# Performance work log

Measured on AMD Instinct MI355X. Metric: run time of the kernel, lower is better.

Reference implementation:

```python
import jax, jax.numpy as jnp
import numpy as np

B, L, C = 16, 2048, 1024
H, G, K = 16, 4, 5
GC = C // G          # group channels = 256
DH = C // H          # head channels = 64
PAD = K // 2         # 2


def conv1d(x, w, b, pad):
    # x: [N, Cin, L], w: [Cout, Cin, K]
    out = jax.lax.conv_general_dilated(x, w, (1,), [(pad, pad)],
                                       dimension_numbers=('NCH', 'OIH', 'NCH'))
    return out + b[None, :, None]


def setup_inputs() -> dict:
    key = jax.random.key(0)
    ks = jax.random.split(key, 16)
    s = 0.02
    inp = {
        'x': jax.random.normal(ks[0], (B, L, C), jnp.float32),
        'Wq': jax.random.normal(ks[1], (C, C), jnp.float32) * s,
        'bq': jnp.zeros((C,), jnp.float32),
        'Wk': jax.random.normal(ks[2], (C, C), jnp.float32) * s,
        'bk': jnp.zeros((C,), jnp.float32),
        'Wv': jax.random.normal(ks[3], (C, C), jnp.float32) * s,
        'bv': jnp.zeros((C,), jnp.float32),
        'Woff1': jax.random.normal(ks[4], (GC, GC, K), jnp.float32) * s,
        'boff1': jnp.zeros((GC,), jnp.float32),
        'Woff2': jax.random.normal(ks[5], (1, GC, 1), jnp.float32) * s,
        'boff2': jnp.zeros((1,), jnp.float32),
        'rpb_table': jax.random.normal(ks[6], (1, C, L), jnp.float32) * 0.02,
        'Wout': jax.random.normal(ks[7], (C, C), jnp.float32) * s,
        'bout': jnp.zeros((C,), jnp.float32),
    }
    return inp


def reference(x, Wq, bq, Wk, bk, Wv, bv, Woff1, boff1, Woff2, boff2,
              rpb_table, Wout, bout):
    xT = jnp.swapaxes(x, 1, 2)                        # [B, C, L]
    # conv1x1 q projection
    q = jnp.einsum('oc,bcl->bol', Wq, xT) + bq[None, :, None]
    gq = q.reshape(B * G, GC, L)                       # grouped queries
    # offset network: conv(k=5, pad=2) -> conv(k=1, pad=2) => length L+4
    h = conv1d(gq, Woff1, boff1, PAD)                  # [BG, GC, L]
    off = conv1d(h, Woff2, boff2, PAD)                 # [BG, 1, L+4]
    off = jnp.tanh(off[:, 0, :]) * K                   # offset_range_factor = kernel
    L4 = L + 2 * PAD
    grid = jnp.arange(L4, dtype=x.dtype)
    vgrid = grid[None, :] + off                        # [BG, L4]
    vs = 2.0 * vgrid / (L4 - 1) - 1.0                  # normalize with n = L+4 (as in source)
    # grid_sample bilinear, align_corners=False, zeros padding, over length L
    pos = ((vs + 1.0) * L - 1.0) / 2.0
    i0 = jnp.floor(pos)
    w1 = pos - i0
    i0 = i0.astype(jnp.int32)
    feats = xT.reshape(B * G, GC, L)

    def gather(idx):
        valid = ((idx >= 0) & (idx < L)).astype(x.dtype)
        idxc = jnp.clip(idx, 0, L - 1)
        g = jnp.take_along_axis(feats, jnp.broadcast_to(idxc[:, None, :], (B * G, GC, L4)), axis=2)
        return g * valid[:, None, :]

    samp = gather(i0) * (1.0 - w1)[:, None, :] + gather(i0 + 1) * w1[:, None, :]
    x_sampled = samp[:, :, :L].reshape(B, C, L)

    k = jnp.einsum('oc,bcl->bol', Wk, x_sampled) + bk[None, :, None]
    v = jnp.einsum('oc,bcl->bol', Wv, x_sampled) + bv[None, :, None] + rpb_table

    qh = q.reshape(B * H, DH, L)
    kh = k.reshape(B * H, DH, L)
    vh = v.reshape(B * H, DH, L)
    # attention over head-channel dims, contracting over sequence (faithful to source)
    scores = jnp.einsum('bil,bjl->bij', qh, kh) * (C ** -0.5)   # [BH, DH, DH]
    attn = jax.nn.softmax(scores, axis=-1)
    out = jnp.einsum('bij,bjl->bil', attn, vh)                  # [BH, DH, L]
    # rearrange '(b g) l c -> b c (g l)' with b=B, g=H, l=DH, c=L
    out = out.reshape(B, H, DH, L).transpose(0, 3, 1, 2).reshape(B, L, C)
    return out @ Wout.T + bout
```

## Files before the change

kernel.cpp:

```cpp
#include <hip/hip_runtime.h>
#include <hip/hip_bf16.h>
#include <stdint.h>

#define BATCH 16
#define SEQ   2048
#define CH    1024
#define NH    16
#define NG    4
#define KW    5
#define GCH   256
#define DHD   64
#define NBG   (BATCH*NG)
#define NBH   (BATCH*NH)
#define MROWS (BATCH*SEQ)

typedef __hip_bfloat16 bf16;
typedef float f32x4 __attribute__((ext_vector_type(4)));
typedef __bf16 bf16x8 __attribute__((ext_vector_type(8)));

__device__ __forceinline__ void unpack8(uint4 r, float* f){
    uint32_t w0=r.x,w1=r.y,w2=r.z,w3=r.w;
    f[0]=__uint_as_float(w0<<16); f[1]=__uint_as_float(w0&0xffff0000u);
    f[2]=__uint_as_float(w1<<16); f[3]=__uint_as_float(w1&0xffff0000u);
    f[4]=__uint_as_float(w2<<16); f[5]=__uint_as_float(w2&0xffff0000u);
    f[6]=__uint_as_float(w3<<16); f[7]=__uint_as_float(w3&0xffff0000u);
}

__global__ __launch_bounds__(256)
void cvt_kernel(const float* __restrict__ in, bf16* __restrict__ out, int n)
{
    int i = (blockIdx.x*256 + threadIdx.x)*8;
    if (i >= n) return;
    float4 f0 = *(const float4*)(in+i);
    float4 f1 = *(const float4*)(in+i+4);
    union { bf16 b[8]; uint4 u; } pk;
    pk.b[0]=__float2bfloat16(f0.x); pk.b[1]=__float2bfloat16(f0.y);
    pk.b[2]=__float2bfloat16(f0.z); pk.b[3]=__float2bfloat16(f0.w);
    pk.b[4]=__float2bfloat16(f1.x); pk.b[5]=__float2bfloat16(f1.y);
    pk.b[6]=__float2bfloat16(f1.z); pk.b[7]=__float2bfloat16(f1.w);
    *(uint4*)(out+i) = pk.u;
}

__global__ void prep_weff_kernel(const float* __restrict__ W1, const float* __restrict__ b1,
                                 const float* __restrict__ w2, const float* __restrict__ b2,
                                 float* __restrict__ weff, float* __restrict__ wcst)
{
    int kk = blockIdx.x;
    int cj = threadIdx.x;
    float s = 0.f;
    for (int co=0; co<GCH; ++co)
        s += w2[co] * W1[((size_t)co*GCH + cj)*KW + kk];
    weff[kk*GCH + cj] = s;
    if (kk==0 && cj==0){
        float sb = 0.f;
        for (int co=0; co<GCH; ++co) sb += w2[co]*b1[co];
        wcst[0] = b2[0];
        wcst[1] = sb;
    }
}

template<int MODE>
__global__ __launch_bounds__(512, 2)
void gemm256_kernel(const bf16* __restrict__ A, const bf16* __restrict__ Wb,
                    const float* __restrict__ bias, const float* __restrict__ rpb,
                    void* __restrict__ outp)
{
    __shared__ __bf16 SM[2*32768];
    const int t = threadIdx.x;
    const int w = t>>6, l = t&63;
    const int wrow = w>>2, wcol = w&3;
    const int lr = l&15, kq = l>>4;

    const int lin = blockIdx.x;
    const int xcd = lin&7, sblk = lin>>3;
    const int m0 = (xcd*16 + (sblk>>2))*256;
    const int n0 = (sblk&3)*256;

    const bf16* Ag = A  + (size_t)m0*CH;
    const bf16* Bg = Wb + (size_t)n0*CH;

    int srow[4], scol[4];
    #pragma unroll
    for (int r=0;r<4;++r){
        int o = (t + 512*r)*16;
        int e = o ^ (((o>>7)&7)<<4);
        srow[r] = e>>7;
        scol[r] = (e&127)>>1;
    }

    auto STAGE = [&](int tile, int buf){
        const int kt = tile*64;
        __bf16* ab = SM + buf*32768;
        __bf16* bb = ab + 16384;
        #pragma unroll
        for (int r=0;r<4;++r){
            __builtin_amdgcn_global_load_lds(
                (const __attribute__((address_space(1))) void*)(Ag + (size_t)srow[r]*CH + kt + scol[r]),
                (__attribute__((address_space(3))) void*)(ab + w*512 + r*4096), 16, 0, 0);
            __builtin_amdgcn_global_load_lds(
                (const __attribute__((address_space(1))) void*)(Bg + (size_t)srow[r]*CH + kt + scol[r]),
                (__attribute__((address_space(3))) void*)(bb + w*512 + r*4096), 16, 0, 0);
        }
    };

    f32x4 acc[8][4];
    #pragma unroll
    for (int i=0;i<8;++i)
        #pragma unroll
        for (int j=0;j<4;++j) acc[i][j] = (f32x4){0.f,0.f,0.f,0.f};

    STAGE(0, 0);
    asm volatile("s_waitcnt vmcnt(0)" ::: "memory");
    __builtin_amdgcn_s_barrier();
    __builtin_amdgcn_sched_barrier(0);

    const int NT = CH/64;
    for (int tt=0; tt<NT; ++tt){
        const int cur = tt&1;
        if (tt+1 < NT) STAGE(tt+1, cur^1);
        __builtin_amdgcn_sched_barrier(0);

        const __bf16* As_ = SM + cur*32768;
        const __bf16* Bs_ = As_ + 16384;
        #pragma unroll
        for (int ks=0; ks<2; ++ks){
            bf16x8 af[8], bfr[4];
            #pragma unroll
            for (int fi=0; fi<8; ++fi){
                int row = wrow*128 + fi*16 + lr;
                int byte = row*128 + ks*64 + kq*16;
                byte ^= (row&7)<<4;
                af[fi] = *(const bf16x8*)(As_ + (byte>>1));
            }
            #pragma unroll
            for (int fj=0; fj<4; ++fj){
                int row = wcol*64 + fj*16 + lr;
                int byte = row*128 + ks*64 + kq*16;
                byte ^= (row&7)<<4;
                bfr[fj] = *(const bf16x8*)(Bs_ + (byte>>1));
            }
            asm volatile("s_waitcnt lgkmcnt(0)" ::: "memory");
            __builtin_amdgcn_sched_barrier(0);
            __builtin_amdgcn_s_setprio(1);
            #pragma unroll
            for (int fi=0; fi<8; ++fi)
                #pragma unroll
                for (int fj=0; fj<4; ++fj)
                    acc[fi][fj] = __builtin_amdgcn_mfma_f32_16x16x32_bf16(af[fi], bfr[fj], acc[fi][fj], 0,0,0);
            __builtin_amdgcn_s_setprio(0);
        }
        asm volatile("s_waitcnt vmcnt(0)" ::: "memory");
        __builtin_amdgcn_s_barrier();
        __builtin_amdgcn_sched_barrier(0);
    }

    float bs[4];
    #pragma unroll
    for (int fj=0;fj<4;++fj) bs[fj] = bias[n0 + wcol*64 + fj*16 + lr];

    if constexpr (MODE == 2){
        const int bb2 = m0 >> 11;
        const int l0g = m0 & (SEQ-1);
        bf16* outT = (bf16*)outp;
        #pragma unroll
        for (int fi=0; fi<8; ++fi){
            int rowl = wrow*128 + fi*16 + kq*4;
            #pragma unroll
            for (int fj=0; fj<4; ++fj){
                int col = n0 + wcol*64 + fj*16 + lr;
                union { bf16 h[4]; uint2 u; } pk;
                #pragma unroll
                for (int r=0;r<4;++r) pk.h[r] = __float2bfloat16(acc[fi][fj][r] + bs[fj]);
                *(uint2*)(outT + ((size_t)(bb2*CH + col))*SEQ + l0g + rowl) = pk.u;
            }
        }
    } else {
        #pragma unroll
        for (int fi=0; fi<8; ++fi){
            #pragma unroll
            for (int r=0;r<4;++r){
                int mg = m0 + wrow*128 + fi*16 + kq*4 + r;
                int lseq = mg & (SEQ-1);
                #pragma unroll
                for (int fj=0; fj<4; ++fj){
                    int ng = n0 + wcol*64 + fj*16 + lr;
                    float v = acc[fi][fj][r] + bs[fj];
                    if constexpr (MODE==1) v += rpb[(size_t)ng*SEQ + lseq];
                    if constexpr (MODE==3)
                        ((float*)outp)[(size_t)mg*CH + ng] = v;
                    else
                        ((bf16*)outp)[(size_t)mg*CH + ng] = __float2bfloat16(v);
                }
            }
        }
    }
}

__global__ __launch_bounds__(256)
void offsets_kernel(const bf16* __restrict__ QT, const float* __restrict__ weff,
                    const float* __restrict__ wcst, float* __restrict__ posb)
{
    __shared__ float P5R[8][272][5];
    __shared__ float weffL[KW][GCH];
    const int t = threadIdx.x;
    const int chunk = blockIdx.x, bg = blockIdx.y;
    const int b = bg>>2, g = bg&3;
    const int l0 = chunk*256;

    for (int i = t; i < KW*GCH; i += 256) weffL[i>>8][i&255] = weff[i];
    __syncthreads();

    const int jg = t & 31, cg = t >> 5;

    auto doblock = [&](int jb, int cgx){
        const int j0 = l0 - 8 + jb*8;
        float acc[8][KW];
        #pragma unroll
        for (int e=0;e<8;++e)
            #pragma unroll
            for (int kk=0;kk<KW;++kk) acc[e][kk] = 0.f;
        const bf16* base = QT + ((size_t)(b*CH + g*GCH + cgx*32))*SEQ;
        const bool safe = (j0 >= 0) && (j0 + 8 <= SEQ);
        if (safe){
            #pragma unroll 4
            for (int i=0;i<32;++i){
                float xv[8];
                { union { bf16x8 v; uint4 u; } cv;
                  cv.v = *(const bf16x8*)(base + (size_t)i*SEQ + j0);
                  unpack8(cv.u, xv); }
                float wk[KW];
                #pragma unroll
                for (int kk=0;kk<KW;++kk) wk[kk] = weffL[kk][cgx*32 + i];
                #pragma unroll
                for (int e=0;e<8;++e)
                    #pragma unroll
                    for (int kk=0;kk<KW;++kk) acc[e][kk] += xv[e]*wk[kk];
            }
        } else {
            for (int i=0;i<32;++i){
                float wk[KW];
                #pragma unroll
                for (int kk=0;kk<KW;++kk) wk[kk] = weffL[kk][cgx*32 + i];
                #pragma unroll
                for (int e=0;e<8;++e){
                    int j = j0 + e;
                    float xv = (j >= 0 && j < SEQ)
                             ? __bfloat162float(base[(size_t)i*SEQ + j]) : 0.f;
                    #pragma unroll
                    for (int kk=0;kk<KW;++kk) acc[e][kk] += xv*wk[kk];
                }
            }
        }
        #pragma unroll
        for (int e=0;e<8;++e)
            #pragma unroll
            for (int kk=0;kk<KW;++kk) P5R[cgx][jb*8+e][kk] = acc[e][kk];
    };

    doblock(jg, cg);
    if (t < 16) doblock(32 + (t&1), t>>1);
    __syncthreads();

    const int lp = l0 + t;
    const float b2 = wcst[0], wb1 = wcst[1];
    float o;
    if (lp < 2){
        o = b2;
    } else {
        float s = b2 + wb1;
        #pragma unroll
        for (int kk=0;kk<KW;++kk){
            int j = lp - 4 + kk;
            if (j >= 0 && j < SEQ){
                int jp = t + 4 + kk;
                float v = 0.f;
                #pragma unroll
                for (int c8=0;c8<8;++c8) v += P5R[c8][jp][kk];
                s += v;
            }
        }
        o = s;
    }
    float off = tanhf(o) * (float)KW;
    posb[bg*SEQ + lp] = ((float)lp + off) * (2048.0f/2051.0f) - 0.5f;
}

__global__ __launch_bounds__(256)
void sample_kernel(const bf16* __restrict__ Xbf, const float* __restrict__ posb,
                   bf16* __restrict__ XS)
{
    const int ci = threadIdx.x, bg = blockIdx.y;
    const int b = bg>>2, g = bg&3;
    const int lp0 = blockIdx.x*8;
    #pragma unroll
    for (int s8=0; s8<8; ++s8){
        int lp = lp0 + s8;
        float p  = posb[bg*SEQ + lp];
        float fl = floorf(p);
        float w1 = p - fl;
        int i0 = (int)fl;
        float v = 0.f;
        if (i0 >= 0 && i0 < SEQ)
            v += __bfloat162float(Xbf[((size_t)(b*SEQ + i0))*CH + g*GCH + ci]) * (1.f - w1);
        if (i0+1 >= 0 && i0+1 < SEQ)
            v += __bfloat162float(Xbf[((size_t)(b*SEQ + i0 + 1))*CH + g*GCH + ci]) * w1;
        XS[((size_t)(b*SEQ + lp))*CH + g*GCH + ci] = __float2bfloat16(v);
    }
}

__global__ __launch_bounds__(256)
void attn_s_kernel(const bf16* __restrict__ QT, const bf16* __restrict__ KT,
                   bf16* __restrict__ Pbuf)
{
    __shared__ float Sc[64][69];
    __shared__ float red[64][4];
    __shared__ float mrow[64];
    __shared__ float sinv[64];
    const int t = threadIdx.x, w = t>>6, l = t&63;
    const int bh = blockIdx.x, b = bh>>4, h = bh&15;
    const bf16* q = QT + ((size_t)(b*CH + h*DHD))*SEQ;
    const bf16* k = KT + ((size_t)(b*CH + h*DHD))*SEQ;
    const int lr = l&15, lk = (l>>4)*8;

    f32x4 acc[4][4];
    #pragma unroll
    for (int i=0;i<4;++i)
        #pragma unroll
        for (int j=0;j<4;++j) acc[i][j] = (f32x4){0.f,0.f,0.f,0.f};

    for (int ks=0; ks<16; ++ks){
        int kp = w*512 + ks*32 + lk;
        bf16x8 af[4], bk8[4];
        #pragma unroll
        for (int i=0;i<4;++i) af[i]  = *(const bf16x8*)(q + (size_t)(i*16+lr)*SEQ + kp);
        #pragma unroll
        for (int j=0;j<4;++j) bk8[j] = *(const bf16x8*)(k + (size_t)(j*16+lr)*SEQ + kp);
        #pragma unroll
        for (int i=0;i<4;++i)
            #pragma unroll
            for (int j=0;j<4;++j)
                acc[i][j] = __builtin_amdgcn_mfma_f32_16x16x32_bf16(af[i], bk8[j], acc[i][j], 0,0,0);
    }
    for (int wv=0; wv<4; ++wv){
        if (w == wv){
            #pragma unroll
            for (int i=0;i<4;++i)
                #pragma unroll
                for (int j=0;j<4;++j)
                    #pragma unroll
                    for (int r=0;r<4;++r){
                        int m = i*16 + (l>>4)*4 + r, n = j*16 + lr;
                        if (wv==0) Sc[m][n]  = acc[i][j][r];
                        else       Sc[m][n] += acc[i][j][r];
                    }
        }
        __syncthreads();
    }
    const int r0 = t & 63, p = t >> 6;
    const float SCALE = 0.03125f;
    float mx = -1e30f;
    #pragma unroll
    for (int c=0;c<16;++c) mx = fmaxf(mx, Sc[r0][p*16+c]*SCALE);
    red[r0][p] = mx;
    __syncthreads();
    if (t < 64) mrow[t] = fmaxf(fmaxf(red[t][0],red[t][1]), fmaxf(red[t][2],red[t][3]));
    __syncthreads();
    float m = mrow[r0], s = 0.f;
    #pragma unroll
    for (int c=0;c<16;++c){
        float e = expf(Sc[r0][p*16+c]*SCALE - m);
        Sc[r0][p*16+c] = e;
        s += e;
    }
    red[r0][p] = s;
    __syncthreads();
    if (t < 64) sinv[t] = 1.f/(red[t][0]+red[t][1]+red[t][2]+red[t][3]);
    __syncthreads();
    float inv = sinv[r0];
    union { bf16 b[8]; uint4 u; } p0, p1;
    #pragma unroll
    for (int e=0;e<8;++e){
        p0.b[e] = __float2bfloat16(Sc[r0][p*16+e]*inv);
        p1.b[e] = __float2bfloat16(Sc[r0][p*16+8+e]*inv);
    }
    bf16* dst = Pbuf + (size_t)bh*4096 + r0*64 + p*16;
    *(uint4*)dst       = p0.u;
    *(uint4*)(dst + 8) = p1.u;
}

__global__ __launch_bounds__(256)
void attn_pv_kernel(const bf16* __restrict__ Pbuf, const bf16* __restrict__ V,
                    bf16* __restrict__ F)
{
    __shared__ __bf16 Pl[64][72];
    const int t = threadIdx.x, w = t>>6, l = t&63;
    const int chunk = blockIdx.x, bh = blockIdx.y;
    const int b = bh>>4, h = bh&15;
    {
        int row = t>>2, coff = (t&3)*16;
        const bf16* src = Pbuf + (size_t)bh*4096 + row*64 + coff;
        *(uint4*)&Pl[row][coff]   = *(const uint4*)src;
        *(uint4*)&Pl[row][coff+8] = *(const uint4*)(src+8);
    }
    __syncthreads();
    const int lr = l&15, lk = (l>>4)*8;
    const int lw = chunk*256 + w*64;

    f32x4 acc[4][4];
    #pragma unroll
    for (int i=0;i<4;++i)
        #pragma unroll
        for (int j=0;j<4;++j) acc[i][j] = (f32x4){0.f,0.f,0.f,0.f};

    #pragma unroll
    for (int ks=0; ks<2; ++ks){
        bf16x8 pf[4], vf[4];
        #pragma unroll
        for (int ni=0;ni<4;++ni) pf[ni] = *(const bf16x8*)&Pl[ni*16+lr][ks*32+lk];
        #pragma unroll
        for (int mi=0;mi<4;++mi)
            vf[mi] = *(const bf16x8*)(V + ((size_t)(b*SEQ + lw + mi*16 + lr))*CH + h*DHD + ks*32 + lk);
        #pragma unroll
        for (int mi=0;mi<4;++mi)
            #pragma unroll
            for (int ni=0;ni<4;++ni)
                acc[mi][ni] = __builtin_amdgcn_mfma_f32_16x16x32_bf16(vf[mi], pf[ni], acc[mi][ni], 0,0,0);
    }
    #pragma unroll
    for (int mi=0;mi<4;++mi){
        #pragma unroll
        for (int r=0;r<4;++r){
            int lpos = lw + mi*16 + (l>>4)*4 + r;
            #pragma unroll
            for (int ni=0;ni<4;++ni)
                F[((size_t)(b*SEQ + lpos))*CH + h*DHD + ni*16 + lr] =
                    __float2bfloat16(acc[mi][ni][r]);
        }
    }
}

extern "C" void kernel_launch(void* const* d_in, const int* in_sizes, int n_in,
                              void* d_out, int out_size, void* d_ws, size_t ws_size,
                              hipStream_t stream)
{
    const float* x   = (const float*)d_in[0];
    const float* Wq  = (const float*)d_in[1];
    const float* bq  = (const float*)d_in[2];
    const float* Wk  = (const float*)d_in[3];
    const float* bk  = (const float*)d_in[4];
    const float* Wv  = (const float*)d_in[5];
    const float* bv  = (const float*)d_in[6];
    const float* W1  = (const float*)d_in[7];
    const float* b1  = (const float*)d_in[8];
    const float* w2  = (const float*)d_in[9];
    const float* b2  = (const float*)d_in[10];
    const float* rpb = (const float*)d_in[11];
    const float* Wo  = (const float*)d_in[12];
    const float* bo  = (const float*)d_in[13];

    char* ws = (char*)d_ws;
    bf16*  Xbf  = (bf16*)(ws);
    bf16*  QT   = (bf16*)(ws + (size_t) 67108864);
    bf16*  XS   = (bf16*)(ws + (size_t)134217728);
    bf16*  VB   = (bf16*)(ws + (size_t)201326592);
    bf16*  Pbuf = (bf16*)(ws + (size_t)268435456);
    bf16*  wslot= (bf16*)(ws + (size_t)270532608);
    float* posb = (float*)(ws + (size_t)272629760);
    float* weff = (float*)(ws + (size_t)273154048);
    float* wcst = (float*)(ws + (size_t)273159168);
    bf16*  KT = Xbf;
    bf16*  Fb = XS;

    prep_weff_kernel<<<dim3(KW), dim3(GCH), 0, stream>>>(W1, b1, w2, b2, weff, wcst);
    cvt_kernel<<<dim3(MROWS*CH/8/256), 256, 0, stream>>>(x, Xbf, MROWS*CH);

    cvt_kernel<<<dim3(CH*CH/8/256), 256, 0, stream>>>(Wq, wslot, CH*CH);
    gemm256_kernel<2><<<dim3(512), 512, 0, stream>>>(Xbf, wslot, bq, nullptr, QT);

    offsets_kernel<<<dim3(SEQ/256, NBG), 256, 0, stream>>>(QT, weff, wcst, posb);
    sample_kernel<<<dim3(SEQ/8, NBG), 256, 0, stream>>>(Xbf, posb, XS);

    cvt_kernel<<<dim3(CH*CH/8/256), 256, 0, stream>>>(Wk, wslot, CH*CH);
    gemm256_kernel<2><<<dim3(512), 512, 0, stream>>>(XS, wslot, bk, nullptr, KT);

    cvt_kernel<<<dim3(CH*CH/8/256), 256, 0, stream>>>(Wv, wslot, CH*CH);
    gemm256_kernel<1><<<dim3(512), 512, 0, stream>>>(XS, wslot, bv, rpb, VB);

    attn_s_kernel<<<dim3(NBH), 256, 0, stream>>>(QT, KT, Pbuf);
    attn_pv_kernel<<<dim3(8, NBH), 256, 0, stream>>>(Pbuf, VB, Fb);

    cvt_kernel<<<dim3(CH*CH/8/256), 256, 0, stream>>>(Wo, wslot, CH*CH);
    gemm256_kernel<3><<<dim3(512), 512, 0, stream>>>(Fb, wslot, bo, nullptr, (float*)d_out);
}
```

Before: 602.6 us.

## Triple-buffer GEMM with K=32 tiles and interleaved split prefetch

Restructures the 256x256 bf16 GEMM main loop from double-buffered K=64 tiles to triple-buffered K=32 tiles with a two-deep prefetch. The prefetch is split into two quarter-stages issued between the two halves of each tile's MFMA work, and vmcnt waits are relaxed so global-to-LDS loads overlap more compute. The LDS swizzle changes to fit the 64-byte rows. This lowers LDS use and memory latency exposure, at the cost of more barriers per K step and smaller MFMA batches between them.

```diff
diff --git a/kernel.cpp b/kernel.cpp
--- a/kernel.cpp
+++ b/kernel.cpp
@@ -65,7 +65,7 @@
                     const float* __restrict__ bias, const float* __restrict__ rpb,
                     void* __restrict__ outp)
 {
-    __shared__ __bf16 SM[2*32768];
+    __shared__ __bf16 SM[3*16384];
     const int t = threadIdx.x;
     const int w = t>>6, l = t&63;
     const int wrow = w>>2, wcol = w&3;
@@ -79,28 +79,25 @@
     const bf16* Ag = A  + (size_t)m0*CH;
     const bf16* Bg = Wb + (size_t)n0*CH;
 
-    int srow[4], scol[4];
-    #pragma unroll
-    for (int r=0;r<4;++r){
+    int srow[2], scol[2];
+    #pragma unroll
+    for (int r=0;r<2;++r){
         int o = (t + 512*r)*16;
-        int e = o ^ (((o>>7)&7)<<4);
-        srow[r] = e>>7;
-        scol[r] = (e&127)>>1;
-    }
-
-    auto STAGE = [&](int tile, int buf){
-        const int kt = tile*64;
-        __bf16* ab = SM + buf*32768;
-        __bf16* bb = ab + 16384;
-        #pragma unroll
-        for (int r=0;r<4;++r){
-            __builtin_amdgcn_global_load_lds(
-                (const __attribute__((address_space(1))) void*)(Ag + (size_t)srow[r]*CH + kt + scol[r]),
-                (__attribute__((address_space(3))) void*)(ab + w*512 + r*4096), 16, 0, 0);
-            __builtin_amdgcn_global_load_lds(
-                (const __attribute__((address_space(1))) void*)(Bg + (size_t)srow[r]*CH + kt + scol[r]),
-                (__attribute__((address_space(3))) void*)(bb + w*512 + r*4096), 16, 0, 0);
-        }
+        int e = o ^ (((o>>7)&3)<<4);
+        srow[r] = e>>6;
+        scol[r] = (e&63)>>1;
+    }
+
+    auto QSTAGE = [&](int tile, int buf, int r){
+        const int kt = tile*32;
+        __bf16* ab = SM + buf*16384;
+        __bf16* bb = ab + 8192;
+        __builtin_amdgcn_global_load_lds(
+            (const __attribute__((address_space(1))) void*)(Ag + (size_t)srow[r]*CH + kt + scol[r]),
+            (__attribute__((address_space(3))) void*)(ab + w*512 + r*4096), 16, 0, 0);
+        __builtin_amdgcn_global_load_lds(
+            (const __attribute__((address_space(1))) void*)(Bg + (size_t)srow[r]*CH + kt + scol[r]),
+            (__attribute__((address_space(3))) void*)(bb + w*512 + r*4096), 16, 0, 0);
     };
 
     f32x4 acc[8][4];
@@ -109,47 +106,67 @@
         #pragma unroll
         for (int j=0;j<4;++j) acc[i][j] = (f32x4){0.f,0.f,0.f,0.f};
 
-    STAGE(0, 0);
-    asm volatile("s_waitcnt vmcnt(0)" ::: "memory");
+    QSTAGE(0,0,0); QSTAGE(0,0,1);
+    QSTAGE(1,1,0); QSTAGE(1,1,1);
+    asm volatile("s_waitcnt vmcnt(4)" ::: "memory");
     __builtin_amdgcn_s_barrier();
     __builtin_amdgcn_sched_barrier(0);
 
-    const int NT = CH/64;
+    const int NT = CH/32;
     for (int tt=0; tt<NT; ++tt){
-        const int cur = tt&1;
-        if (tt+1 < NT) STAGE(tt+1, cur^1);
+        const int cur = tt%3, nxt = (tt+2)%3;
+        const bool pf = (tt+2 < NT);
+        const __bf16* As_ = SM + cur*16384;
+        const __bf16* Bs_ = As_ + 8192;
+        bf16x8 af[4], bfr[4];
+
+        #pragma unroll
+        for (int fi=0; fi<4; ++fi){
+            int row = wrow*128 + fi*16 + lr;
+            int o = row*64 + kq*16;
+            o ^= ((o>>7)&3)<<4;
+            af[fi] = *(const bf16x8*)(As_ + (o>>1));
+        }
+        #pragma unroll
+        for (int fj=0; fj<4; ++fj){
+            int row = wcol*64 + fj*16 + lr;
+            int o = row*64 + kq*16;
+            o ^= ((o>>7)&3)<<4;
+            bfr[fj] = *(const bf16x8*)(Bs_ + (o>>1));
+        }
+        if (pf) QSTAGE(tt+2, nxt, 0);
+        __builtin_amdgcn_s_barrier();
+        asm volatile("s_waitcnt lgkmcnt(0)" ::: "memory");
         __builtin_amdgcn_sched_barrier(0);
-
-        const __bf16* As_ = SM + cur*32768;
-        const __bf16* Bs_ = As_ + 16384;
-        #pragma unroll
-        for (int ks=0; ks<2; ++ks){
-            bf16x8 af[8], bfr[4];
-            #pragma unroll
-            for (int fi=0; fi<8; ++fi){
-                int row = wrow*128 + fi*16 + lr;
-                int byte = row*128 + ks*64 + kq*16;
-                byte ^= (row&7)<<4;
-                af[fi] = *(const bf16x8*)(As_ + (byte>>1));
-            }
-            #pragma unroll
-            for (int fj=0; fj<4; ++fj){
-                int row = wcol*64 + fj*16 + lr;
-                int byte = row*128 + ks*64 + kq*16;
-                byte ^= (row&7)<<4;
-                bfr[fj] = *(const bf16x8*)(Bs_ + (byte>>1));
-            }
-            asm volatile("s_waitcnt lgkmcnt(0)" ::: "memory");
-            __builtin_amdgcn_sched_barrier(0);
-            __builtin_amdgcn_s_setprio(1);
-            #pragma unroll
-            for (int fi=0; fi<8; ++fi)
-                #pragma unroll
-                for (int fj=0; fj<4; ++fj)
-                    acc[fi][fj] = __builtin_amdgcn_mfma_f32_16x16x32_bf16(af[fi], bfr[fj], acc[fi][fj], 0,0,0);
-            __builtin_amdgcn_s_setprio(0);
-        }
-        asm volatile("s_waitcnt vmcnt(0)" ::: "memory");
+        __builtin_amdgcn_s_setprio(1);
+        #pragma unroll
+        for (int fi=0; fi<4; ++fi)
+            #pragma unroll
+            for (int fj=0; fj<4; ++fj)
+                acc[fi][fj] = __builtin_amdgcn_mfma_f32_16x16x32_bf16(af[fi], bfr[fj], acc[fi][fj], 0,0,0);
+        __builtin_amdgcn_s_setprio(0);
+        __builtin_amdgcn_s_barrier();
+
+        #pragma unroll
+        for (int fi=0; fi<4; ++fi){
+            int row = wrow*128 + (fi+4)*16 + lr;
+            int o = row*64 + kq*16;
+            o ^= ((o>>7)&3)<<4;
+            af[fi] = *(const bf16x8*)(As_ + (o>>1));
+        }
+        if (pf) QSTAGE(tt+2, nxt, 1);
+        __builtin_amdgcn_s_barrier();
+        asm volatile("s_waitcnt lgkmcnt(0)" ::: "memory");
+        __builtin_amdgcn_sched_barrier(0);
+        __builtin_amdgcn_s_setprio(1);
+        #pragma unroll
+        for (int fi=0; fi<4; ++fi)
+            #pragma unroll
+            for (int fj=0; fj<4; ++fj)
+                acc[fi+4][fj] = __builtin_amdgcn_mfma_f32_16x16x32_bf16(af[fi], bfr[fj], acc[fi+4][fj], 0,0,0);
+        __builtin_amdgcn_s_setprio(0);
+        if (pf) asm volatile("s_waitcnt vmcnt(4)" ::: "memory");
+        else    asm volatile("s_waitcnt vmcnt(0)" ::: "memory");
         __builtin_amdgcn_s_barrier();
         __builtin_amdgcn_sched_barrier(0);
     }
```

Measured after the change: 619.7 us. 2.8% more time.

## Fuse attention softmax and PV kernels; drop GEMM scheduling barriers

Applied to the files above, without the earlier changes.

Merges the score/softmax kernel and the PV kernel into one kernel per head that keeps the probability matrix in LDS and loops over sequence chunks, removing the Pbuf round-trip and a launch. It also strips sched_barrier, setprio and the per-kstep LDS wait from the main GEMM loop, leaving instruction scheduling to the compiler. The fused kernel launches far fewer blocks for the memory-heavy PV phase, reducing parallelism, and the GEMM may lose its tuned overlap.

```diff
diff --git a/kernel.cpp b/kernel.cpp
--- a/kernel.cpp
+++ b/kernel.cpp
@@ -112,7 +112,6 @@
     STAGE(0, 0);
     asm volatile("s_waitcnt vmcnt(0)" ::: "memory");
     __builtin_amdgcn_s_barrier();
-    __builtin_amdgcn_sched_barrier(0);
 
     const int NT = CH/64;
     for (int tt=0; tt<NT; ++tt){
@@ -139,19 +138,15 @@
                 byte ^= (row&7)<<4;
                 bfr[fj] = *(const bf16x8*)(Bs_ + (byte>>1));
             }
-            asm volatile("s_waitcnt lgkmcnt(0)" ::: "memory");
-            __builtin_amdgcn_sched_barrier(0);
-            __builtin_amdgcn_s_setprio(1);
             #pragma unroll
             for (int fi=0; fi<8; ++fi)
                 #pragma unroll
                 for (int fj=0; fj<4; ++fj)
                     acc[fi][fj] = __builtin_amdgcn_mfma_f32_16x16x32_bf16(af[fi], bfr[fj], acc[fi][fj], 0,0,0);
-            __builtin_amdgcn_s_setprio(0);
-        }
+        }
+        asm volatile("s_waitcnt lgkmcnt(0)" ::: "memory");
         asm volatile("s_waitcnt vmcnt(0)" ::: "memory");
         __builtin_amdgcn_s_barrier();
-        __builtin_amdgcn_sched_barrier(0);
     }
 
     float bs[4];
@@ -309,13 +304,14 @@
 }
 
 __global__ __launch_bounds__(256)
-void attn_s_kernel(const bf16* __restrict__ QT, const bf16* __restrict__ KT,
-                   bf16* __restrict__ Pbuf)
+void attn_fused_kernel(const bf16* __restrict__ QT, const bf16* __restrict__ KT,
+                       const bf16* __restrict__ V, bf16* __restrict__ F)
 {
     __shared__ float Sc[64][69];
     __shared__ float red[64][4];
     __shared__ float mrow[64];
     __shared__ float sinv[64];
+    __shared__ __bf16 Pl[64][72];
     const int t = threadIdx.x, w = t>>6, l = t&63;
     const int bh = blockIdx.x, b = bh>>4, h = bh&15;
     const bf16* q = QT + ((size_t)(b*CH + h*DHD))*SEQ;
@@ -377,64 +373,48 @@
     if (t < 64) sinv[t] = 1.f/(red[t][0]+red[t][1]+red[t][2]+red[t][3]);
     __syncthreads();
     float inv = sinv[r0];
-    union { bf16 b[8]; uint4 u; } p0, p1;
-    #pragma unroll
-    for (int e=0;e<8;++e){
-        p0.b[e] = __float2bfloat16(Sc[r0][p*16+e]*inv);
-        p1.b[e] = __float2bfloat16(Sc[r0][p*16+8+e]*inv);
-    }
-    bf16* dst = Pbuf + (size_t)bh*4096 + r0*64 + p*16;
-    *(uint4*)dst       = p0.u;
-    *(uint4*)(dst + 8) = p1.u;
-}
-
-__global__ __launch_bounds__(256)
-void attn_pv_kernel(const bf16* __restrict__ Pbuf, const bf16* __restrict__ V,
-                    bf16* __restrict__ F)
-{
-    __shared__ __bf16 Pl[64][72];
-    const int t = threadIdx.x, w = t>>6, l = t&63;
-    const int chunk = blockIdx.x, bh = blockIdx.y;
-    const int b = bh>>4, h = bh&15;
-    {
-        int row = t>>2, coff = (t&3)*16;
-        const bf16* src = Pbuf + (size_t)bh*4096 + row*64 + coff;
-        *(uint4*)&Pl[row][coff]   = *(const uint4*)src;
-        *(uint4*)&Pl[row][coff+8] = *(const uint4*)(src+8);
-    }
-    __syncthreads();
-    const int lr = l&15, lk = (l>>4)*8;
-    const int lw = chunk*256 + w*64;
-
-    f32x4 acc[4][4];
-    #pragma unroll
-    for (int i=0;i<4;++i)
-        #pragma unroll
-        for (int j=0;j<4;++j) acc[i][j] = (f32x4){0.f,0.f,0.f,0.f};
-
-    #pragma unroll
-    for (int ks=0; ks<2; ++ks){
-        bf16x8 pf[4], vf[4];
-        #pragma unroll
-        for (int ni=0;ni<4;++ni) pf[ni] = *(const bf16x8*)&Pl[ni*16+lr][ks*32+lk];
-        #pragma unroll
-        for (int mi=0;mi<4;++mi)
-            vf[mi] = *(const bf16x8*)(V + ((size_t)(b*SEQ + lw + mi*16 + lr))*CH + h*DHD + ks*32 + lk);
-        #pragma unroll
-        for (int mi=0;mi<4;++mi)
-            #pragma unroll
-            for (int ni=0;ni<4;++ni)
-                acc[mi][ni] = __builtin_amdgcn_mfma_f32_16x16x32_bf16(vf[mi], pf[ni], acc[mi][ni], 0,0,0);
-    }
-    #pragma unroll
-    for (int mi=0;mi<4;++mi){
-        #pragma unroll
-        for (int r=0;r<4;++r){
-            int lpos = lw + mi*16 + (l>>4)*4 + r;
-            #pragma unroll
-            for (int ni=0;ni<4;++ni)
-                F[((size_t)(b*SEQ + lpos))*CH + h*DHD + ni*16 + lr] =
-                    __float2bfloat16(acc[mi][ni][r]);
+    #pragma unroll
+    for (int e=0;e<16;++e)
+        Pl[r0][p*16+e] = (__bf16)__float2bfloat16(Sc[r0][p*16+e]*inv);
+    __syncthreads();
+
+    const size_t base = (size_t)b*SEQ*CH + (size_t)h*DHD;
+    bf16x8 pf[4][2];
+    #pragma unroll
+    for (int ks=0; ks<2; ++ks)
+        #pragma unroll
+        for (int ni=0;ni<4;++ni)
+            pf[ni][ks] = *(const bf16x8*)&Pl[ni*16+lr][ks*32+lk];
+
+    for (int c8=0; c8<8; ++c8){
+        const int lw = c8*256 + w*64;
+        f32x4 po[4][4];
+        #pragma unroll
+        for (int i=0;i<4;++i)
+            #pragma unroll
+            for (int j=0;j<4;++j) po[i][j] = (f32x4){0.f,0.f,0.f,0.f};
+        #pragma unroll
+        for (int ks=0; ks<2; ++ks){
+            bf16x8 vf[4];
+            #pragma unroll
+            for (int mi=0;mi<4;++mi)
+                vf[mi] = *(const bf16x8*)(V + base + (size_t)(lw + mi*16 + lr)*CH + h*0 + ks*32 + lk);
+            #pragma unroll
+            for (int mi=0;mi<4;++mi)
+                #pragma unroll
+                for (int ni=0;ni<4;++ni)
+                    po[mi][ni] = __builtin_amdgcn_mfma_f32_16x16x32_bf16(vf[mi], pf[ni][ks], po[mi][ni], 0,0,0);
+        }
+        #pragma unroll
+        for (int mi=0;mi<4;++mi){
+            #pragma unroll
+            for (int r=0;r<4;++r){
+                int lpos = lw + mi*16 + (l>>4)*4 + r;
+                #pragma unroll
+                for (int ni=0;ni<4;++ni)
+                    F[base + (size_t)lpos*CH + ni*16 + lr] =
+                        __float2bfloat16(po[mi][ni][r]);
+            }
         }
     }
 }
@@ -463,7 +443,6 @@
     bf16*  QT   = (bf16*)(ws + (size_t) 67108864);
     bf16*  XS   = (bf16*)(ws + (size_t)134217728);
     bf16*  VB   = (bf16*)(ws + (size_t)201326592);
-    bf16*  Pbuf = (bf16*)(ws + (size_t)268435456);
     bf16*  wslot= (bf16*)(ws + (size_t)270532608);
     float* posb = (float*)(ws + (size_t)272629760);
     float* weff = (float*)(ws + (size_t)273154048);
@@ -486,8 +465,7 @@
     cvt_kernel<<<dim3(CH*CH/8/256), 256, 0, stream>>>(Wv, wslot, CH*CH);
     gemm256_kernel<1><<<dim3(512), 512, 0, stream>>>(XS, wslot, bv, rpb, VB);
 
-    attn_s_kernel<<<dim3(NBH), 256, 0, stream>>>(QT, KT, Pbuf);
-    attn_pv_kernel<<<dim3(8, NBH), 256, 0, stream>>>(Pbuf, VB, Fb);
+    attn_fused_kernel<<<dim3(NBH), 256, 0, stream>>>(QT, KT, VB, Fb);
 
     cvt_kernel<<<dim3(CH*CH/8/256), 256, 0, stream>>>(Wo, wslot, CH*CH);
     gemm256_kernel<3><<<dim3(512), 512, 0, stream>>>(Fb, wslot, bo, nullptr, (float*)d_out);
```

Result: no change. 593.4 us (-1.5%).
